# Optimization experiments

Hardware: AMD Instinct MI355X
Metric: run time of the kernel (lower is better)

Reference implementation:

```python
import jax, jax.numpy as jnp
import numpy as np
from jax import lax

SPATIAL = 4
DN = ('NCHW', 'OIHW', 'NCHW')

def setup_inputs() -> dict:
    key = jax.random.key(0)
    ks = jax.random.split(key, 6)
    b, c_in, h, w = 32, 256, 56, 56
    c_out, kk, n_exp, red = 256, 3, 3, 16
    fan = c_in * kk * kk
    return {
        'x': jax.random.normal(ks[0], (b, c_in, h, w), jnp.float32),
        'w_expert': jax.random.normal(ks[1], (n_exp, c_out, c_in, kk, kk), jnp.float32) / np.sqrt(fan),
        'route_conv_w': jax.random.normal(ks[2], (red, c_in), jnp.float32) / np.sqrt(c_in),
        'route_conv_b': jax.random.normal(ks[3], (red,), jnp.float32) * 0.05,
        'fc_w': jax.random.normal(ks[4], (n_exp, red * SPATIAL * SPATIAL), jnp.float32) / np.sqrt(red * SPATIAL * SPATIAL),
        'fc_b': jax.random.normal(ks[5], (n_exp,), jnp.float32) * 0.05,
    }

def _routing(x, route_conv_w, route_conv_b, fc_w, fc_b):
    b, c, h, w = x.shape
    # AdaptiveAvgPool2d(4): h, w divisible by 4 -> exact block mean
    pooled = x.reshape(b, c, SPATIAL, h // SPATIAL, SPATIAL, w // SPATIAL).mean(axis=(3, 5))  # [b,c,4,4]
    r = jnp.einsum('bcij,rc->brij', pooled, route_conv_w) + route_conv_b[None, :, None, None]
    r = jax.nn.relu(r).reshape(b, -1)                         # [b, red*16]
    r = jax.nn.relu(r @ fc_w.T + fc_b)                        # [b, n_exp]
    return jax.nn.sigmoid(r)

def reference(x, w_expert, route_conv_w, route_conv_b, fc_w, fc_b):
    rw = _routing(x, route_conv_w, route_conv_b, fc_w, fc_b)              # [b,k]
    cw = jnp.einsum('bk,koihw->boihw', rw, w_expert)                      # per-sample mixed weights
    def conv1(xi, wi):
        return lax.conv_general_dilated(xi[None], wi, window_strides=(1, 1),
                                        padding=[(1, 1), (1, 1)],
                                        dimension_numbers=DN)[0]
    return jax.vmap(conv1)(x, cw)  # [b, c_out, h, w]
```

## Files before the change

### kernel.cpp

```cpp
#include <hip/hip_runtime.h>
#include <hip/hip_bf16.h>
#include <stdint.h>

#define NB   32
#define CIN  256
#define COUT 256
#define WW   56
#define HW   3136
#define NEXP 3
#define KTOT 2304
#define XP   58
#define XPP  3364
#define NKT  36

typedef __attribute__((ext_vector_type(8))) __bf16 bf16x8;
typedef __attribute__((ext_vector_type(4))) float  f32x4;

#define OFF_RW     0
#define OFF_POOLED 1024
#define OFF_CWT    (1024 + 32*256*16*4)
#define CWT_BYTES  ((size_t)NB*COUT*KTOT*2)
#define OFF_XPAD   (OFF_CWT + CWT_BYTES)

#define PRE_XPAD 6272
#define PRE_POOL 8192
#define PRE_NBLK (PRE_XPAD + PRE_POOL + NB)

__global__ __launch_bounds__(256) void k_pre(const float* __restrict__ x,
                                             float* __restrict__ pooled,
                                             __bf16* __restrict__ xpad) {
    __shared__ __align__(16) char smem[8448];
    int blk = blockIdx.x;
    int t = threadIdx.x;

    if (blk < PRE_XPAD) {
        int pt = blk % 49;
        int r2 = blk / 49;
        int ct = r2 & 3;
        int b  = r2 >> 2;
        __bf16 (*lds)[66] = (__bf16(*)[66])smem;
        int pl = t & 63;
        int cb = t >> 6;
        const float* xb = x + ((size_t)(b * CIN + ct * 64)) * HW + pt * 64;
        #pragma unroll
        for (int ic = 0; ic < 16; ++ic) {
            int cl = ic * 4 + cb;
            lds[cl][pl] = (__bf16)xb[(size_t)cl * HW + pl];
        }
        __syncthreads();
        #pragma unroll
        for (int iw = 0; iw < 2; ++iw) {
            int idx = iw * 256 + t;
            int p_l = idx >> 3, c8 = (idx & 7) * 8;
            int p = pt * 64 + p_l;
            int y = p / WW, xx = p - y * WW;
            union { __bf16 h[8]; uint4 u; } pk;
            #pragma unroll
            for (int j = 0; j < 8; ++j) pk.h[j] = lds[c8 + j][p_l];
            __bf16* dst = xpad + ((size_t)b * XPP + (y + 1) * XP + (xx + 1)) * CIN
                          + ct * 64 + c8;
            *(uint4*)dst = pk.u;
        }
    } else if (blk < PRE_XPAD + PRE_POOL) {
        int j = blk - PRE_XPAD;
        int b = j >> 8, c = j & 255;
        float (*lds)[56] = (float(*)[56])smem;
        const float* xb = x + ((size_t)(b * CIN + c)) * HW;
        if (t < 224) {
            int xc = t % 56, yg = t / 56;
            const float* p = xb + (yg * 14) * WW + xc;
            float s = 0.f;
            #pragma unroll
            for (int r = 0; r < 14; ++r) s += p[r * WW];
            lds[yg][xc] = s;
        }
        __syncthreads();
        if (t < 16) {
            int sy = t >> 2, sx = t & 3;
            float s = 0.f;
            #pragma unroll
            for (int jj = 0; jj < 14; ++jj) s += lds[sy][sx * 14 + jj];
            pooled[(((size_t)b * CIN + c) << 4) + t] = s * (1.f / 196.f);
        }
    } else {
        int b = blk - (PRE_XPAD + PRE_POOL);
        for (int idx = t; idx < 228 * 32; idx += 256) {
            int pos = idx >> 5;
            int co = (idx & 31) * 8;
            int yy, xx;
            if (pos < 58)       { yy = 0;          xx = pos; }
            else if (pos < 116) { yy = 57;         xx = pos - 58; }
            else if (pos < 172) { yy = pos - 115;  xx = 0; }
            else                { yy = pos - 171;  xx = 57; }
            uint4 z = {0u, 0u, 0u, 0u};
            *(uint4*)(xpad + ((size_t)b * XPP + yy * XP + xx) * CIN + co) = z;
        }
    }
}

__global__ __launch_bounds__(256) void k_route(const float* __restrict__ pooled,
                                               const float* __restrict__ rcw,
                                               const float* __restrict__ rcb,
                                               const float* __restrict__ fcw,
                                               const float* __restrict__ fcb,
                                               float* __restrict__ rw) {
    int b = blockIdx.x;
    int t = threadIdx.x;
    int r = t >> 4, ij = t & 15;
    __shared__ float rbuf[256];
    const float* pb = pooled + (size_t)b * CIN * 16;
    float acc = rcb[r];
    for (int c = 0; c < CIN; ++c)
        acc += pb[c * 16 + ij] * rcw[r * CIN + c];
    rbuf[t] = fmaxf(acc, 0.f);
    __syncthreads();
    if (t < NEXP) {
        float a = fcb[t];
        for (int f = 0; f < 256; ++f) a += rbuf[f] * fcw[t * 256 + f];
        a = fmaxf(a, 0.f);
        rw[b * NEXP + t] = 1.f / (1.f + expf(-a));
    }
}

__global__ __launch_bounds__(256) void k_mixw(const float* __restrict__ we,
                                              const float* __restrict__ rw,
                                              __bf16* __restrict__ cwt) {
    int o = blockIdx.x;
    int i = threadIdx.x;
    float wv[3][9];
    #pragma unroll
    for (int e = 0; e < 3; ++e) {
        const float* p = we + (((size_t)e * COUT + o) * CIN + i) * 9;
        #pragma unroll
        for (int k = 0; k < 9; ++k) wv[e][k] = p[k];
    }
    for (int b = 0; b < NB; ++b) {
        float r0 = rw[b * 3 + 0], r1 = rw[b * 3 + 1], r2 = rw[b * 3 + 2];
        __bf16* op = cwt + ((size_t)(b * COUT + o)) * KTOT + i;
        #pragma unroll
        for (int k = 0; k < 9; ++k) {
            float v = r0 * wv[0][k] + r1 * wv[1][k] + r2 * wv[2][k];
            op[k * 256] = (__bf16)v;
        }
    }
}

#define GL16(g, l) __builtin_amdgcn_global_load_lds( \
    (const __attribute__((address_space(1))) uint32_t*)(g), \
    (__attribute__((address_space(3))) uint32_t*)(l), 16, 0, 0)

#define STAGE_A(o, kh, aoffn) do { \
    GL16(gA0 + (aoffn) + (kh)*64, LDS + (o)*32768 + (kh)*16384 +     0 + wid*1024); \
    GL16(gA1 + (aoffn) + (kh)*64, LDS + (o)*32768 + (kh)*16384 +  4096 + wid*1024); \
    GL16(gA2 + (aoffn) + (kh)*64, LDS + (o)*32768 + (kh)*16384 +  8192 + wid*1024); \
    GL16(gA3 + (aoffn) + (kh)*64, LDS + (o)*32768 + (kh)*16384 + 12288 + wid*1024); \
  } while (0)
#define STAGE_B(o, kh, boffn) do { \
    GL16(gB0 + (boffn) + (kh)*64, LDS + 65536 + (o)*32768 + (kh)*16384 +     0 + wid*1024); \
    GL16(gB1 + (boffn) + (kh)*64, LDS + 65536 + (o)*32768 + (kh)*16384 +  4096 + wid*1024); \
    GL16(gB2 + (boffn) + (kh)*64, LDS + 65536 + (o)*32768 + (kh)*16384 +  8192 + wid*1024); \
    GL16(gB3 + (boffn) + (kh)*64, LDS + 65536 + (o)*32768 + (kh)*16384 + 12288 + wid*1024); \
  } while (0)

#define BARRIER() do { \
    __builtin_amdgcn_sched_barrier(0); \
    __builtin_amdgcn_s_barrier(); \
    __builtin_amdgcn_sched_barrier(0); \
  } while (0)
#define VMCNT(n) do { \
    asm volatile("s_waitcnt vmcnt(" #n ")" ::: "memory"); \
    __builtin_amdgcn_sched_barrier(0); \
  } while (0)
#define LGKM0() do { \
    asm volatile("s_waitcnt lgkmcnt(0)" ::: "memory"); \
    __builtin_amdgcn_sched_barrier(0); \
  } while (0)

#define LOAD8(F, base) do { \
    F[0] = *(const bf16x8*)((base) + 0); \
    F[1] = *(const bf16x8*)((base) + 1024); \
    F[2] = *(const bf16x8*)((base) + 2048); \
    F[3] = *(const bf16x8*)((base) + 3072); \
    F[4] = *(const bf16x8*)((base) + 4096); \
    F[5] = *(const bf16x8*)((base) + 5120); \
    F[6] = *(const bf16x8*)((base) + 6144); \
    F[7] = *(const bf16x8*)((base) + 7168); \
  } while (0)
#define MMALL() do { \
    __builtin_amdgcn_s_setprio(1); \
    _Pragma("unroll") \
    for (int mf = 0; mf < 8; ++mf) \
      _Pragma("unroll") \
      for (int nf = 0; nf < 8; ++nf) \
        acc[mf][nf] = __builtin_amdgcn_mfma_f32_16x16x32_bf16( \
            af[mf], bq[nf], acc[mf][nf], 0, 0, 0); \
    __builtin_amdgcn_s_setprio(0); \
  } while (0)

#define HALF(c, o, kh, aoffn, boffn) do { \
    VMCNT(8); \
    BARRIER(); \
    { const char* aCur = LDS + (c)*32768 + (kh)*16384 + aRd; \
      const char* bCur = LDS + 65536 + (c)*32768 + (kh)*16384 + bRd; \
      LOAD8(af, aCur); \
      LOAD8(bq, bCur); } \
    STAGE_A(o, kh, aoffn); \
    STAGE_B(o, kh, boffn); \
    LGKM0(); \
    MMALL(); \
  } while (0)

__global__ __launch_bounds__(256, 1) void k_conv(const __bf16* __restrict__ cwt,
                                                 const __bf16* __restrict__ xpad,
                                                 float* __restrict__ out) {
    extern __shared__ __align__(16) char LDS[];

    int flat = blockIdx.x;
    int logical = (flat & 7) * 52 + (flat >> 3);
    int b  = logical / 13;
    int nt = logical - b * 13;

    int tid = threadIdx.x;
    int ln  = tid & 63;
    int wid = tid >> 6;
    int wr  = wid >> 1;
    int wc  = wid & 1;
    int fr  = ln & 15;
    int kw  = ln >> 4;
    int xsw = ((fr >> 1) & 3) << 4;

    const char *gA0, *gA1, *gA2, *gA3, *gB0, *gB1, *gB2, *gB3;
    {
        const char* cwb = (const char*)(cwt + (size_t)b * COUT * KTOT);
        const char* xpb = (const char*)(xpad + (size_t)b * XPP * CIN);
        #pragma unroll
        for (int i = 0; i < 4; ++i) {
            int L = i * 4096 + wid * 1024 + ln * 16;
            int U = L ^ (((L >> 7) & 3) << 4);
            int rowU = U >> 6;
            int kbU  = U & 63;
            const char* ga = cwb + (size_t)rowU * (KTOT * 2) + kbU;
            int p = nt * 256 + rowU; if (p > HW - 1) p = HW - 1;
            int y = p / WW, x = p - y * WW;
            const char* gb = xpb + (size_t)(y * XP + x) * (CIN * 2) + kbU;
            if (i == 0)      { gA0 = ga; gB0 = gb; }
            else if (i == 1) { gA1 = ga; gB1 = gb; }
            else if (i == 2) { gA2 = ga; gB2 = gb; }
            else             { gA3 = ga; gB3 = gb; }
        }
    }

    int aRd = (wr * 128 + fr) * 64 + ((kw * 16) ^ xsw);
    int bRd = (wc * 128 + fr) * 64 + ((kw * 16) ^ xsw);

    f32x4 acc[8][8];
    #pragma unroll
    for (int i = 0; i < 8; ++i)
        #pragma unroll
        for (int j = 0; j < 8; ++j)
            acc[i][j] = (f32x4){0.f, 0.f, 0.f, 0.f};

    bf16x8 af[8], bq[8];

    STAGE_A(0, 0, 0);
    STAGE_B(0, 0, 0);
    STAGE_A(0, 1, 0);
    STAGE_B(0, 1, 0);

    for (int kt = 0; kt < NKT - 1; ++kt) {
        int c = kt & 1, o = c ^ 1;
        int ktn  = kt + 1;
        int aoffn = ktn * 128;
        int ktap = ktn >> 2;
        int kyn  = (ktap * 11) >> 5;
        int kxn  = ktap - kyn * 3;
        int boffn = (kyn * XP + kxn) * 512 + (ktn & 3) * 128;

        HALF(c, o, 0, aoffn, boffn);
        HALF(c, o, 1, aoffn, boffn);
    }

    {
        VMCNT(0);
        BARRIER();
        const char* aCur = LDS + 32768 + aRd;
        const char* bCur = LDS + 65536 + 32768 + bRd;
        LOAD8(af, aCur); LOAD8(bq, bCur);
        LGKM0();
        MMALL();
        aCur += 16384; bCur += 16384;
        LOAD8(af, aCur); LOAD8(bq, bCur);
        LGKM0();
        MMALL();
    }

    float* ob = out + ((size_t)(b * COUT + wr * 128)) * HW;
    int colbase = nt * 256 + wc * 128;
    int rb = (ln >> 4) * 4;
    #pragma unroll
    for (int nf = 0; nf < 8; ++nf) {
        int col = colbase + nf * 16 + fr;
        if (col < HW) {
            #pragma unroll
            for (int mf = 0; mf < 8; ++mf)
                #pragma unroll
                for (int r = 0; r < 4; ++r)
                    ob[(size_t)(mf * 16 + rb + r) * HW + col] = acc[mf][nf][r];
        }
    }
}

extern "C" void kernel_launch(void* const* d_in, const int* in_sizes, int n_in,
                              void* d_out, int out_size, void* d_ws, size_t ws_size,
                              hipStream_t stream) {
    (void)in_sizes; (void)n_in; (void)out_size; (void)ws_size;
    const float* x   = (const float*)d_in[0];
    const float* we  = (const float*)d_in[1];
    const float* rcw = (const float*)d_in[2];
    const float* rcb = (const float*)d_in[3];
    const float* fcw = (const float*)d_in[4];
    const float* fcb = (const float*)d_in[5];
    float* out = (float*)d_out;

    char* ws = (char*)d_ws;
    float*  rw     = (float*)(ws + OFF_RW);
    float*  pooled = (float*)(ws + OFF_POOLED);
    __bf16* cwt    = (__bf16*)(ws + OFF_CWT);
    __bf16* xpad   = (__bf16*)(ws + OFF_XPAD);

    (void)hipFuncSetAttribute((const void*)k_conv,
                              hipFuncAttributeMaxDynamicSharedMemorySize, 131072);

    k_pre<<<PRE_NBLK, 256, 0, stream>>>(x, pooled, xpad);
    k_route<<<NB, 256, 0, stream>>>(pooled, rcw, rcb, fcw, fcb, rw);
    k_mixw<<<COUT, 256, 0, stream>>>(we, rw, cwt);
    k_conv<<<416, 256, 131072, stream>>>(cwt, xpad, out);
}
```

Before: 204.4 us.

## Split conv block tile across 16 waves with 64x64 per-wave subtiles

```diff
diff --git a/kernel.cpp b/kernel.cpp
--- a/kernel.cpp
+++ b/kernel.cpp
@@ -149,18 +149,10 @@
     (const __attribute__((address_space(1))) uint32_t*)(g), \
     (__attribute__((address_space(3))) uint32_t*)(l), 16, 0, 0)
 
-#define STAGE_A(o, kh, aoffn) do { \
-    GL16(gA0 + (aoffn) + (kh)*64, LDS + (o)*32768 + (kh)*16384 +     0 + wid*1024); \
-    GL16(gA1 + (aoffn) + (kh)*64, LDS + (o)*32768 + (kh)*16384 +  4096 + wid*1024); \
-    GL16(gA2 + (aoffn) + (kh)*64, LDS + (o)*32768 + (kh)*16384 +  8192 + wid*1024); \
-    GL16(gA3 + (aoffn) + (kh)*64, LDS + (o)*32768 + (kh)*16384 + 12288 + wid*1024); \
-  } while (0)
-#define STAGE_B(o, kh, boffn) do { \
-    GL16(gB0 + (boffn) + (kh)*64, LDS + 65536 + (o)*32768 + (kh)*16384 +     0 + wid*1024); \
-    GL16(gB1 + (boffn) + (kh)*64, LDS + 65536 + (o)*32768 + (kh)*16384 +  4096 + wid*1024); \
-    GL16(gB2 + (boffn) + (kh)*64, LDS + 65536 + (o)*32768 + (kh)*16384 +  8192 + wid*1024); \
-    GL16(gB3 + (boffn) + (kh)*64, LDS + 65536 + (o)*32768 + (kh)*16384 + 12288 + wid*1024); \
-  } while (0)
+#define STAGE_A(o, kh, aoffn) \
+    GL16(gA + (aoffn) + (kh)*64, LDS + (o)*32768 + (kh)*16384 + wid*1024)
+#define STAGE_B(o, kh, boffn) \
+    GL16(gB + (boffn) + (kh)*64, LDS + 65536 + (o)*32768 + (kh)*16384 + wid*1024)
 
 #define BARRIER() do { \
     __builtin_amdgcn_sched_barrier(0); \
@@ -176,43 +168,39 @@
     __builtin_amdgcn_sched_barrier(0); \
   } while (0)
 
-#define LOAD8(F, base) do { \
+#define LOAD4(F, base) do { \
     F[0] = *(const bf16x8*)((base) + 0); \
     F[1] = *(const bf16x8*)((base) + 1024); \
     F[2] = *(const bf16x8*)((base) + 2048); \
     F[3] = *(const bf16x8*)((base) + 3072); \
-    F[4] = *(const bf16x8*)((base) + 4096); \
-    F[5] = *(const bf16x8*)((base) + 5120); \
-    F[6] = *(const bf16x8*)((base) + 6144); \
-    F[7] = *(const bf16x8*)((base) + 7168); \
   } while (0)
 #define MMALL() do { \
     __builtin_amdgcn_s_setprio(1); \
     _Pragma("unroll") \
-    for (int mf = 0; mf < 8; ++mf) \
+    for (int mf = 0; mf < 4; ++mf) \
       _Pragma("unroll") \
-      for (int nf = 0; nf < 8; ++nf) \
+      for (int nf = 0; nf < 4; ++nf) \
         acc[mf][nf] = __builtin_amdgcn_mfma_f32_16x16x32_bf16( \
             af[mf], bq[nf], acc[mf][nf], 0, 0, 0); \
     __builtin_amdgcn_s_setprio(0); \
   } while (0)
 
 #define HALF(c, o, kh, aoffn, boffn) do { \
-    VMCNT(8); \
+    VMCNT(2); \
     BARRIER(); \
     { const char* aCur = LDS + (c)*32768 + (kh)*16384 + aRd; \
       const char* bCur = LDS + 65536 + (c)*32768 + (kh)*16384 + bRd; \
-      LOAD8(af, aCur); \
-      LOAD8(bq, bCur); } \
+      LOAD4(af, aCur); \
+      LOAD4(bq, bCur); } \
     STAGE_A(o, kh, aoffn); \
     STAGE_B(o, kh, boffn); \
     LGKM0(); \
     MMALL(); \
   } while (0)
 
-__global__ __launch_bounds__(256, 1) void k_conv(const __bf16* __restrict__ cwt,
-                                                 const __bf16* __restrict__ xpad,
-                                                 float* __restrict__ out) {
+__global__ __launch_bounds__(1024, 4) void k_conv(const __bf16* __restrict__ cwt,
+                                                  const __bf16* __restrict__ xpad,
+                                                  float* __restrict__ out) {
     extern __shared__ __align__(16) char LDS[];
 
     int flat = blockIdx.x;
@@ -223,44 +211,37 @@
     int tid = threadIdx.x;
     int ln  = tid & 63;
     int wid = tid >> 6;
-    int wr  = wid >> 1;
-    int wc  = wid & 1;
+    int wr  = wid >> 2;
+    int wc  = wid & 3;
     int fr  = ln & 15;
     int kw  = ln >> 4;
     int xsw = ((fr >> 1) & 3) << 4;
 
-    const char *gA0, *gA1, *gA2, *gA3, *gB0, *gB1, *gB2, *gB3;
+    const char *gA, *gB;
     {
         const char* cwb = (const char*)(cwt + (size_t)b * COUT * KTOT);
         const char* xpb = (const char*)(xpad + (size_t)b * XPP * CIN);
-        #pragma unroll
-        for (int i = 0; i < 4; ++i) {
-            int L = i * 4096 + wid * 1024 + ln * 16;
-            int U = L ^ (((L >> 7) & 3) << 4);
-            int rowU = U >> 6;
-            int kbU  = U & 63;
-            const char* ga = cwb + (size_t)rowU * (KTOT * 2) + kbU;
-            int p = nt * 256 + rowU; if (p > HW - 1) p = HW - 1;
-            int y = p / WW, x = p - y * WW;
-            const char* gb = xpb + (size_t)(y * XP + x) * (CIN * 2) + kbU;
-            if (i == 0)      { gA0 = ga; gB0 = gb; }
-            else if (i == 1) { gA1 = ga; gB1 = gb; }
-            else if (i == 2) { gA2 = ga; gB2 = gb; }
-            else             { gA3 = ga; gB3 = gb; }
-        }
-    }
-
-    int aRd = (wr * 128 + fr) * 64 + ((kw * 16) ^ xsw);
-    int bRd = (wc * 128 + fr) * 64 + ((kw * 16) ^ xsw);
-
-    f32x4 acc[8][8];
+        int L = tid * 16;
+        int U = L ^ (((L >> 7) & 3) << 4);
+        int rowU = U >> 6;
+        int kbU  = U & 63;
+        gA = cwb + (size_t)rowU * (KTOT * 2) + kbU;
+        int p = nt * 256 + rowU; if (p > HW - 1) p = HW - 1;
+        int y = p / WW, x = p - y * WW;
+        gB = xpb + (size_t)(y * XP + x) * (CIN * 2) + kbU;
+    }
+
+    int aRd = (wr * 64 + fr) * 64 + ((kw * 16) ^ xsw);
+    int bRd = (wc * 64 + fr) * 64 + ((kw * 16) ^ xsw);
+
+    f32x4 acc[4][4];
     #pragma unroll
-    for (int i = 0; i < 8; ++i)
-        #pragma unroll
-        for (int j = 0; j < 8; ++j)
+    for (int i = 0; i < 4; ++i)
+        #pragma unroll
+        for (int j = 0; j < 4; ++j)
             acc[i][j] = (f32x4){0.f, 0.f, 0.f, 0.f};
 
-    bf16x8 af[8], bq[8];
+    bf16x8 af[4], bq[4];
 
     STAGE_A(0, 0, 0);
     STAGE_B(0, 0, 0);
@@ -285,24 +266,24 @@
         BARRIER();
         const char* aCur = LDS + 32768 + aRd;
         const char* bCur = LDS + 65536 + 32768 + bRd;
-        LOAD8(af, aCur); LOAD8(bq, bCur);
+        LOAD4(af, aCur); LOAD4(bq, bCur);
         LGKM0();
         MMALL();
         aCur += 16384; bCur += 16384;
-        LOAD8(af, aCur); LOAD8(bq, bCur);
+        LOAD4(af, aCur); LOAD4(bq, bCur);
         LGKM0();
         MMALL();
     }
 
-    float* ob = out + ((size_t)(b * COUT + wr * 128)) * HW;
-    int colbase = nt * 256 + wc * 128;
+    float* ob = out + ((size_t)(b * COUT + wr * 64)) * HW;
+    int colbase = nt * 256 + wc * 64;
     int rb = (ln >> 4) * 4;
     #pragma unroll
-    for (int nf = 0; nf < 8; ++nf) {
+    for (int nf = 0; nf < 4; ++nf) {
         int col = colbase + nf * 16 + fr;
         if (col < HW) {
             #pragma unroll
-            for (int mf = 0; mf < 8; ++mf)
+            for (int mf = 0; mf < 4; ++mf)
                 #pragma unroll
                 for (int r = 0; r < 4; ++r)
                     ob[(size_t)(mf * 16 + rb + r) * HW + col] = acc[mf][nf][r];
@@ -334,5 +315,5 @@
     k_pre<<<PRE_NBLK, 256, 0, stream>>>(x, pooled, xpad);
     k_route<<<NB, 256, 0, stream>>>(pooled, rcw, rcb, fcw, fcb, rw);
     k_mixw<<<COUT, 256, 0, stream>>>(we, rw, cwt);
-    k_conv<<<416, 256, 131072, stream>>>(cwt, xpad, out);
-}
+    k_conv<<<416, 1024, 131072, stream>>>(cwt, xpad, out);
+}
```

Result: faster. 199.2 us (-2.6%).
